# Kernel tuning notes

Hardware: AMD Instinct MI355X
Metric: run time of the kernel (lower is better)

The kernel has to match this reference:

```python
import jax, jax.numpy as jnp
import numpy as np
from jax import lax

NEG = -1e16  # value used by masked_fill in the original
DN = ('NCHW', 'OIHW', 'NCHW')


def _time_block(X, w1, b1, w2, b2, w3, b3):
    # X: [B, N, T, C] -> conv over time with kernel (1,3), VALID -> [B, N, T-2, O]
    x = jnp.transpose(X, (0, 3, 1, 2))  # [B, C, N, T]
    conv = lambda w, b: lax.conv_general_dilated(x, w, (1, 1), 'VALID', dimension_numbers=DN) + b[None, :, None, None]
    temp = conv(w1, b1) + jax.nn.sigmoid(conv(w2, b2))
    out = jax.nn.relu(temp + conv(w3, b3))
    return jnp.transpose(out, (0, 2, 3, 1))  # [B, N, T-2, O]


def _gat_single(x, graph, W, b):
    # x: [B, N, C]; W: [D, C]; b: [D]
    h = jnp.einsum('bnc,dc->bnd', x, W)
    s = jnp.einsum('bnd,bmd->bnm', h, h) * graph[None]
    s = jnp.where(s == 0, NEG, s)
    a = jax.nn.softmax(s, axis=-1)
    return jnp.einsum('bnm,bmd->bnd', a, h) + b


def _gat_multihead(x, graph, Wh, bh):
    # x: [B, N, C]; Wh: [H, D, C]; bh: [H, D] -> [B, N, H*D] (head-major concat, matching torch.cat)
    h = jnp.einsum('bnc,hdc->bhnd', x, Wh)
    s = jnp.einsum('bhnd,bhmd->bhnm', h, h) * graph[None, None]
    s = jnp.where(s == 0, NEG, s)
    a = jax.nn.softmax(s, axis=-1)
    o = jnp.einsum('bhnm,bhmd->bhnd', a, h) + bh[None, :, None, :]
    B, H, N, D = o.shape
    return jnp.transpose(o, (0, 2, 1, 3)).reshape(B, N, H * D)


def setup_inputs() -> dict:
    key = jax.random.key(0)
    ks = jax.random.split(key, 12)
    B, N, T, C = 2, 4096, 5, 192
    hid, out_c, H = 64, 64, 4
    inp = {
        'flow': jax.random.normal(ks[0], (B, N, T, C), jnp.float32),
        'graph': jax.random.randint(ks[1], (N, N), 0, 2).astype(jnp.float32),
        'tb_w1': jax.random.normal(ks[2], (hid, C, 1, 3), jnp.float32) * 0.1,
        'tb_b1': jax.random.normal(ks[3], (hid,), jnp.float32) * 0.1,
        'tb_w2': jax.random.normal(ks[4], (hid, C, 1, 3), jnp.float32) * 0.1,
        'tb_b2': jax.random.normal(ks[5], (hid,), jnp.float32) * 0.1,
        'tb_w3': jax.random.normal(ks[6], (hid, C, 1, 3), jnp.float32) * 0.1,
        'tb_b3': jax.random.normal(ks[7], (hid,), jnp.float32) * 0.1,
        'Wh': jax.random.normal(ks[8], (H, hid, C), jnp.float32) * 0.1,
        'bh': jax.random.normal(ks[9], (H, hid), jnp.float32) * 0.1,
        'Wo': jax.random.normal(ks[10], (out_c, hid * H), jnp.float32) * 0.1,
        'bo': jax.random.normal(ks[11], (out_c,), jnp.float32) * 0.1,
    }
    return inp


def reference(flow, graph, tb_w1, tb_b1, tb_w2, tb_b2, tb_w3, tb_b3, Wh, bh, Wo, bo):
    B, N = flow.shape[0], flow.shape[1]
    t1 = _time_block(flow, tb_w1, tb_b1, tb_w2, tb_b2, tb_w3, tb_b3)  # [B, N, T-2, hid]
    x = t1.reshape(B, N, -1)  # [B, N, (T-2)*hid]
    x = jax.nn.leaky_relu(_gat_multihead(x, graph, Wh, bh), negative_slope=0.01)
    x = jax.nn.leaky_relu(_gat_single(x, graph, Wo, bo), negative_slope=0.01)
    return x[:, :, None, :]  # [B, N, 1, out_c]
```

## Files before the change

kernel.cpp:

```cpp
#include <hip/hip_runtime.h>
#include <math.h>

#define N_NODES 4096

typedef unsigned short u16;
typedef unsigned int u32;

typedef __attribute__((ext_vector_type(8))) short bfrag;
typedef __attribute__((ext_vector_type(4))) float f4;

__device__ __forceinline__ u16 f2bf(float x) {
    union { float f; u32 u; } v; v.f = x;
    u32 r = (v.u + 0x7FFFu + ((v.u >> 16) & 1u)) >> 16;
    return (u16)r;
}
__device__ __forceinline__ float bf2f(u16 b) {
    union { float f; u32 u; } v; v.u = ((u32)b) << 16; return v.f;
}
__device__ __forceinline__ u32 cvtpk(float a, float b) {
    u32 r;
    asm("v_cvt_pk_bf16_f32 %0, %1, %2" : "=v"(r) : "v"(a), "v"(b));
    return r;
}
__device__ __forceinline__ float u2f(u32 u) {
    union { u32 u; float f; } v; v.u = u; return v.f;
}
__device__ __forceinline__ float fexp2(float x) {
    float r;
    asm("v_exp_f32 %0, %1" : "=v"(r) : "v"(x));
    return r;
}

#define LOG2E 1.4426950408889634f

__global__ __launch_bounds__(256) void wprep_kernel(
    const float* __restrict__ w1, const float* __restrict__ w2,
    const float* __restrict__ w3,
    u16* __restrict__ w_hi, u16* __restrict__ w_mid, u16* __restrict__ w_lo)
{
    int idx = blockIdx.x * 256 + threadIdx.x;
    if (idx >= 192 * 576) return;
    int col = idx / 576, k = idx % 576;
    int conv = col >> 6, o = col & 63;
    int kk = k / 192, c = k % 192;
    const float* w = (conv == 0) ? w1 : (conv == 1 ? w2 : w3);
    float v = w[(o * 192 + c) * 3 + kk];
    u16 h = f2bf(v);   float r1 = v - bf2f(h);
    u16 m = f2bf(r1);  float r2 = r1 - bf2f(m);
    u16 lo = f2bf(r2);
    int kc = k >> 6, rem = k & 63, j = rem >> 3, e = rem & 7;
    int pos = col * 576 + kc * 64 + ((j ^ (col & 7)) << 3) + e;
    w_hi[pos] = h;
    w_mid[pos] = m;
    w_lo[pos] = lo;
}

__global__ __launch_bounds__(512) void timeblock_mfma_kernel(
    const float* __restrict__ flow,
    const u16* __restrict__ w_hi, const u16* __restrict__ w_mid,
    const u16* __restrict__ w_lo,
    const float* __restrict__ b1, const float* __restrict__ b2,
    const float* __restrict__ b3, float* __restrict__ x1)
{
    __shared__ __align__(16) u16 As[3][128 * 64];
    __shared__ __align__(16) u16 Bs[3][192 * 64];

    const int tid = threadIdx.x;
    const int wv = tid >> 6, l = tid & 63;
    const int ln15 = l & 15, ln16 = l >> 4;
    const int wr = wv >> 1, wc = wv & 1;
    const int nodebase = blockIdx.x * 128;
    const int t = blockIdx.y;

    f4 acc[2][6];
#pragma unroll
    for (int rq = 0; rq < 2; ++rq)
#pragma unroll
        for (int nt = 0; nt < 6; ++nt) {
            acc[rq][nt][0] = 0.f; acc[rq][nt][1] = 0.f;
            acc[rq][nt][2] = 0.f; acc[rq][nt][3] = 0.f;
        }

    for (int kc = 0; kc < 9; ++kc) {
        __syncthreads();

#pragma unroll
        for (int u = tid; u < 1024; u += 512) {
            int r = u >> 3, j = u & 7;
            const float* srcp = flow + (size_t)(nodebase + r) * 960 + t * 192 + kc * 64 + j * 8;
            float4 f0 = *(const float4*)srcp;
            float4 f1 = *(const float4*)(srcp + 4);
            float fv[8] = { f0.x, f0.y, f0.z, f0.w, f1.x, f1.y, f1.z, f1.w };
            union { uint4 q; u16 a[8]; } uh, um, ul;
#pragma unroll
            for (int e = 0; e < 8; ++e) {
                u16 h = f2bf(fv[e]);   float r1 = fv[e] - bf2f(h);
                u16 m = f2bf(r1);      float r2 = r1 - bf2f(m);
                uh.a[e] = h; um.a[e] = m; ul.a[e] = f2bf(r2);
            }
            int pos = r * 64 + ((j ^ (r & 7)) << 3);
            *(uint4*)&As[0][pos] = uh.q;
            *(uint4*)&As[1][pos] = um.q;
            *(uint4*)&As[2][pos] = ul.q;
        }

#pragma unroll
        for (int arr = 0; arr < 3; ++arr) {
            const u16* wsrc = (arr == 0) ? w_hi : (arr == 1 ? w_mid : w_lo);
#pragma unroll
            for (int i = 0; i < 3; ++i) {
                int colg = wv * 24 + i * 8;
                const u16* srcp = wsrc + (size_t)(colg + (l >> 3)) * 576 + kc * 64 + (l & 7) * 8;
                u16* dstp = &Bs[arr][colg * 64];
                __builtin_amdgcn_global_load_lds(
                    (const __attribute__((address_space(1))) u32*)srcp,
                    (__attribute__((address_space(3))) u32*)dstp, 16, 0, 0);
            }
        }

        __syncthreads();

        bfrag af[2][3][2];
#pragma unroll
        for (int rq = 0; rq < 2; ++rq) {
            int arow = wr * 32 + rq * 16 + ln15;
#pragma unroll
            for (int ks = 0; ks < 2; ++ks) {
                int idx = arow * 64 + (((ks * 4 + ln16) ^ (arow & 7)) << 3);
                af[rq][0][ks] = *(const bfrag*)&As[0][idx];
                af[rq][1][ks] = *(const bfrag*)&As[1][idx];
                af[rq][2][ks] = *(const bfrag*)&As[2][idx];
            }
        }

#pragma unroll
        for (int cv = 0; cv < 3; ++cv) {
#pragma unroll
            for (int ntj = 0; ntj < 2; ++ntj) {
                int col = cv * 64 + wc * 32 + ntj * 16 + ln15;
                int nt = cv * 2 + ntj;
#pragma unroll
                for (int ks = 0; ks < 2; ++ks) {
                    int idx = col * 64 + (((ks * 4 + ln16) ^ (col & 7)) << 3);
                    bfrag bh = *(const bfrag*)&Bs[0][idx];
                    bfrag bm = *(const bfrag*)&Bs[1][idx];
                    bfrag bl = *(const bfrag*)&Bs[2][idx];
#pragma unroll
                    for (int rq = 0; rq < 2; ++rq) {
                        f4 a = acc[rq][nt];
                        a = __builtin_amdgcn_mfma_f32_16x16x32_bf16(af[rq][0][ks], bh, a, 0, 0, 0);
                        a = __builtin_amdgcn_mfma_f32_16x16x32_bf16(af[rq][0][ks], bm, a, 0, 0, 0);
                        a = __builtin_amdgcn_mfma_f32_16x16x32_bf16(af[rq][1][ks], bh, a, 0, 0, 0);
                        a = __builtin_amdgcn_mfma_f32_16x16x32_bf16(af[rq][0][ks], bl, a, 0, 0, 0);
                        a = __builtin_amdgcn_mfma_f32_16x16x32_bf16(af[rq][2][ks], bh, a, 0, 0, 0);
                        a = __builtin_amdgcn_mfma_f32_16x16x32_bf16(af[rq][1][ks], bm, a, 0, 0, 0);
                        acc[rq][nt] = a;
                    }
                }
            }
        }
    }

#pragma unroll
    for (int rq = 0; rq < 2; ++rq) {
#pragma unroll
        for (int ntj = 0; ntj < 2; ++ntj) {
            int o = wc * 32 + ntj * 16 + ln15;
            float bb1 = b1[o], bb2 = b2[o], bb3 = b3[o];
#pragma unroll
            for (int rg = 0; rg < 4; ++rg) {
                int node = nodebase + wr * 32 + rq * 16 + ln16 * 4 + rg;
                float c1 = acc[rq][0 * 2 + ntj][rg] + bb1;
                float c2 = acc[rq][1 * 2 + ntj][rg] + bb2;
                float c3 = acc[rq][2 * 2 + ntj][rg] + bb3;
                float sg = 1.0f / (1.0f + __expf(-c2));
                float v = c1 + sg + c3;
                x1[(size_t)node * 192 + t * 64 + o] = v > 0.f ? v : 0.f;
            }
        }
    }
}

__global__ __launch_bounds__(256) void linear64_split_kernel(
    const float* __restrict__ in, const float* __restrict__ W,
    u16* __restrict__ h_hi, u16* __restrict__ h_lo,
    u16* __restrict__ hTb_hi, u16* __restrict__ hTb_lo,
    int C, int H)
{
    __shared__ float xs[64][68];
    __shared__ float wsm[64][68];
    const int tid = threadIdx.x;
    const int g = blockIdx.y;
    const int rowbase = blockIdx.x * 64;
    const int rgrp = tid >> 4, cgrp = tid & 15;

    float acc[4][4] = {};
    for (int c0 = 0; c0 < C; c0 += 64) {
        __syncthreads();
        for (int i = tid; i < 4096; i += 256) {
            int r = i >> 6, cc = i & 63;
            xs[r][cc]  = in[(size_t)(rowbase + r) * C + c0 + cc];
            wsm[r][cc] = W[(size_t)(g * 64 + r) * C + c0 + cc];
        }
        __syncthreads();
        for (int cc = 0; cc < 64; cc += 4) {
            float4 xv[4], wv[4];
#pragma unroll
            for (int i = 0; i < 4; ++i)
                xv[i] = *reinterpret_cast<const float4*>(&xs[4 * rgrp + i][cc]);
#pragma unroll
            for (int j = 0; j < 4; ++j)
                wv[j] = *reinterpret_cast<const float4*>(&wsm[4 * cgrp + j][cc]);
#pragma unroll
            for (int i = 0; i < 4; ++i) {
#pragma unroll
                for (int j = 0; j < 4; ++j) {
                    acc[i][j] += xv[i].x * wv[j].x + xv[i].y * wv[j].y
                               + xv[i].z * wv[j].z + xv[i].w * wv[j].w;
                }
            }
        }
    }

    u16 hi[4][4], lo[4][4];
#pragma unroll
    for (int i = 0; i < 4; ++i)
#pragma unroll
        for (int j = 0; j < 4; ++j) {
            float a = acc[i][j];
            u16 h = f2bf(a);
            hi[i][j] = h;
            lo[i][j] = f2bf(a - bf2f(h));
        }

    const int b = rowbase >> 12;
    const size_t mapb = (size_t)(b * H + g) * (4096 * 64);

#pragma unroll
    for (int i = 0; i < 4; ++i) {
        int n = (rowbase & 4095) + 4 * rgrp + i;
        ushort4 vh = { hi[i][0], hi[i][1], hi[i][2], hi[i][3] };
        ushort4 vl = { lo[i][0], lo[i][1], lo[i][2], lo[i][3] };
        *(ushort4*)&h_hi[mapb + (size_t)n * 64 + 4 * cgrp] = vh;
        *(ushort4*)&h_lo[mapb + (size_t)n * 64 + 4 * cgrp] = vl;
    }
    {
        int n0 = (rowbase & 4095) + 4 * rgrp;
        size_t tb = mapb + ((size_t)(n0 >> 6) * 64) * 64;
#pragma unroll
        for (int j = 0; j < 4; ++j) {
            int d = 4 * cgrp + j;
            ushort4 vh = { hi[0][j], hi[1][j], hi[2][j], hi[3][j] };
            ushort4 vl = { lo[0][j], lo[1][j], lo[2][j], lo[3][j] };
            *(ushort4*)&hTb_hi[tb + (size_t)d * 64 + (n0 & 63)] = vh;
            *(ushort4*)&hTb_lo[tb + (size_t)d * 64 + (n0 & 63)] = vl;
        }
    }
}

__global__ __launch_bounds__(256) void flash_mfma_kernel(
    const u16* __restrict__ h_hi, const u16* __restrict__ h_lo,
    const u16* __restrict__ hTb_hi, const u16* __restrict__ hTb_lo,
    const float* __restrict__ graph, const float* __restrict__ bias,
    float* __restrict__ out, int H, int rstride,
    int ntiles, int nch, int mode, float* __restrict__ pO, float* __restrict__ pml)
{
    __shared__ __align__(16) u16 Ks[2][2][4096];
    __shared__ __align__(16) u16 Vs[2][4096];

    const int tid = threadIdx.x;
    const int wv = tid >> 6;
    const int l = tid & 63;
    const int ln15 = l & 15, ln16 = l >> 4;
    const int bx = blockIdx.y;
    const int by = bx / nch;
    const int chunk = bx - by * nch;
    const int t0 = chunk * ntiles;
    const int bb = by / H, head = by - bb * H;
    const size_t mapb = (size_t)by * (4096 * 64);
    const int rowbase = blockIdx.x * 64;

    const int arow = rowbase + wv * 16 + ln15;
    bfrag ahi[2], alo[2];
#pragma unroll
    for (int ks = 0; ks < 2; ++ks) {
        ahi[ks] = *(const bfrag*)(h_hi + mapb + (size_t)arow * 64 + ks * 32 + ln16 * 8);
        alo[ks] = *(const bfrag*)(h_lo + mapb + (size_t)arow * 64 + ks * 32 + ln16 * 8);
    }

    const u16* gA = (wv == 0 ? h_hi : wv == 1 ? h_lo : wv == 2 ? hTb_hi : hTb_lo) + mapb;
    const int lrow = l >> 3;
    const int stoff = lrow * 64 + (((l & 7) ^ lrow) << 3);

#define STAGE_K(T, BUF)                                                        \
    if (wv < 2) {                                                              \
        const u16* srcp = gA + (size_t)(T) * 4096 + stoff;                     \
        u16* dstp = &Ks[BUF][wv][0];                                           \
        _Pragma("unroll")                                                      \
        for (int i_ = 0; i_ < 8; ++i_)                                         \
            __builtin_amdgcn_global_load_lds(                                  \
                (const __attribute__((address_space(1))) u32*)(srcp + i_ * 512), \
                (__attribute__((address_space(3))) u32*)(dstp + i_ * 512),     \
                16, 0, 0);                                                     \
    }
#define STAGE_V(T)                                                             \
    if (wv >= 2) {                                                             \
        const u16* srcp = gA + (size_t)(T) * 4096 + stoff;                     \
        u16* dstp = &Vs[wv - 2][0];                                            \
        _Pragma("unroll")                                                      \
        for (int i_ = 0; i_ < 8; ++i_)                                         \
            __builtin_amdgcn_global_load_lds(                                  \
                (const __attribute__((address_space(1))) u32*)(srcp + i_ * 512), \
                (__attribute__((address_space(3))) u32*)(dstp + i_ * 512),     \
                16, 0, 0);                                                     \
    }

    const float* grow = graph + (size_t)(rowbase + wv * 16 + ln15) * 4096 + ln16 * 4;

    float m_ = -3.0e38f, l_ = 0.f;
    f4 acco[4];
#pragma unroll
    for (int i = 0; i < 4; ++i) {
        acco[i][0] = 0.f; acco[i][1] = 0.f; acco[i][2] = 0.f; acco[i][3] = 0.f;
    }

    STAGE_K(t0, 0);
    float4 grC[4], grN[4];
#pragma unroll
    for (int cb = 0; cb < 4; ++cb)
        grC[cb] = *(const float4*)(grow + (size_t)t0 * 64 + cb * 16);

    const int srcA = ln15 + ((((ln16 << 1)) & 3) << 4);
    const int srcB = ln15 + ((((ln16 << 1) + 1) & 3) << 4);
    const bool hi2 = (ln16 & 2) != 0;

    for (int tt = 0; tt < ntiles; ++tt) {
        const int t = t0 + tt;
        const int cur = tt & 1;

        __syncthreads();

        STAGE_V(t);
        if (tt + 1 < ntiles) {
            STAGE_K(t + 1, cur ^ 1);
#pragma unroll
            for (int cb = 0; cb < 4; ++cb)
                grN[cb] = *(const float4*)(grow + (size_t)(t + 1) * 64 + cb * 16);
        }

        __builtin_amdgcn_s_setprio(1);
        f4 accs[4];
#pragma unroll
        for (int cb = 0; cb < 4; ++cb) {
            f4 a; a[0] = 0.f; a[1] = 0.f; a[2] = 0.f; a[3] = 0.f;
#pragma unroll
            for (int ks = 0; ks < 2; ++ks) {
                int c = cb * 16 + ln15;
                int idx = c * 64 + (((ks * 4 + ln16) * 8) ^ ((c & 7) << 3));
                bfrag bhi = *(const bfrag*)&Ks[cur][0][idx];
                bfrag blo = *(const bfrag*)&Ks[cur][1][idx];
                a = __builtin_amdgcn_mfma_f32_16x16x32_bf16(bhi, ahi[ks], a, 0, 0, 0);
                a = __builtin_amdgcn_mfma_f32_16x16x32_bf16(bhi, alo[ks], a, 0, 0, 0);
                a = __builtin_amdgcn_mfma_f32_16x16x32_bf16(blo, ahi[ks], a, 0, 0, 0);
            }
            accs[cb] = a;
        }
        __builtin_amdgcn_s_setprio(0);

        float p[4][4];
#pragma unroll
        for (int cb = 0; cb < 4; ++cb) {
            p[cb][0] = accs[cb][0] + fmaf(grC[cb].x, 1e16f, -1e16f);
            p[cb][1] = accs[cb][1] + fmaf(grC[cb].y, 1e16f, -1e16f);
            p[cb][2] = accs[cb][2] + fmaf(grC[cb].z, 1e16f, -1e16f);
            p[cb][3] = accs[cb][3] + fmaf(grC[cb].w, 1e16f, -1e16f);
        }

        float tm = fmaxf(fmaxf(p[0][0], p[0][1]), fmaxf(p[0][2], p[0][3]));
#pragma unroll
        for (int cb = 1; cb < 4; ++cb)
            tm = fmaxf(tm, fmaxf(fmaxf(p[cb][0], p[cb][1]), fmaxf(p[cb][2], p[cb][3])));
        tm = fmaxf(tm, __shfl_xor(tm, 16));
        tm = fmaxf(tm, __shfl_xor(tm, 32));

        const bool anyup = __any(tm > m_);
        float mn, corr;
        if (anyup) {
            mn = fmaxf(m_, tm);
            corr = fexp2((m_ - mn) * LOG2E);
        } else {
            mn = m_;
            corr = 1.0f;
        }
        const float c0 = -mn * LOG2E;

        float rs = 0.f;
#pragma unroll
        for (int cb = 0; cb < 4; ++cb) {
            p[cb][0] = fexp2(fmaf(p[cb][0], LOG2E, c0));
            p[cb][1] = fexp2(fmaf(p[cb][1], LOG2E, c0));
            p[cb][2] = fexp2(fmaf(p[cb][2], LOG2E, c0));
            p[cb][3] = fexp2(fmaf(p[cb][3], LOG2E, c0));
            rs += (p[cb][0] + p[cb][1]) + (p[cb][2] + p[cb][3]);
        }
        rs += __shfl_xor(rs, 16);
        rs += __shfl_xor(rs, 32);
        l_ = l_ * corr + rs;
        m_ = mn;

        if (anyup) {
            float corr4[4];
#pragma unroll
            for (int rg = 0; rg < 4; ++rg)
                corr4[rg] = __shfl(corr, ln16 * 4 + rg);
#pragma unroll
            for (int nb = 0; nb < 4; ++nb) {
                acco[nb][0] *= corr4[0]; acco[nb][1] *= corr4[1];
                acco[nb][2] *= corr4[2]; acco[nb][3] *= corr4[3];
            }
        }

        u32 Uh[4][2], Ul[4][2];
#pragma unroll
        for (int cb = 0; cb < 4; ++cb) {
            u32 uh0 = cvtpk(p[cb][0], p[cb][1]);
            u32 uh1 = cvtpk(p[cb][2], p[cb][3]);
            float h0 = u2f(uh0 << 16), h1 = u2f(uh0 & 0xffff0000u);
            float h2 = u2f(uh1 << 16), h3 = u2f(uh1 & 0xffff0000u);
            Uh[cb][0] = uh0; Uh[cb][1] = uh1;
            Ul[cb][0] = cvtpk(p[cb][0] - h0, p[cb][1] - h1);
            Ul[cb][1] = cvtpk(p[cb][2] - h2, p[cb][3] - h3);
        }

        bfrag pfh[2], pfl[2];
#pragma unroll
        for (int ks = 0; ks < 2; ++ks) {
            u32 w0a = (u32)__shfl((int)Uh[2 * ks + 0][0], srcA);
            u32 w0b = (u32)__shfl((int)Uh[2 * ks + 1][0], srcA);
            u32 w1a = (u32)__shfl((int)Uh[2 * ks + 0][1], srcA);
            u32 w1b = (u32)__shfl((int)Uh[2 * ks + 1][1], srcA);
            u32 w2a = (u32)__shfl((int)Uh[2 * ks + 0][0], srcB);
            u32 w2b = (u32)__shfl((int)Uh[2 * ks + 1][0], srcB);
            u32 w3a = (u32)__shfl((int)Uh[2 * ks + 0][1], srcB);
            u32 w3b = (u32)__shfl((int)Uh[2 * ks + 1][1], srcB);
            union { uint4 q; bfrag f; } ch;
            ch.q.x = hi2 ? w0b : w0a; ch.q.y = hi2 ? w1b : w1a;
            ch.q.z = hi2 ? w2b : w2a; ch.q.w = hi2 ? w3b : w3a;
            pfh[ks] = ch.f;

            u32 v0a = (u32)__shfl((int)Ul[2 * ks + 0][0], srcA);
            u32 v0b = (u32)__shfl((int)Ul[2 * ks + 1][0], srcA);
            u32 v1a = (u32)__shfl((int)Ul[2 * ks + 0][1], srcA);
            u32 v1b = (u32)__shfl((int)Ul[2 * ks + 1][1], srcA);
            u32 v2a = (u32)__shfl((int)Ul[2 * ks + 0][0], srcB);
            u32 v2b = (u32)__shfl((int)Ul[2 * ks + 1][0], srcB);
            u32 v3a = (u32)__shfl((int)Ul[2 * ks + 0][1], srcB);
            u32 v3b = (u32)__shfl((int)Ul[2 * ks + 1][1], srcB);
            union { uint4 q; bfrag f; } cl;
            cl.q.x = hi2 ? v0b : v0a; cl.q.y = hi2 ? v1b : v1a;
            cl.q.z = hi2 ? v2b : v2a; cl.q.w = hi2 ? v3b : v3a;
            pfl[ks] = cl.f;
        }

        __syncthreads();

        __builtin_amdgcn_s_setprio(1);
#pragma unroll
        for (int nb = 0; nb < 4; ++nb) {
#pragma unroll
            for (int ks = 0; ks < 2; ++ks) {
                int nr = nb * 16 + ln15;
                int idx = nr * 64 + (((ks * 4 + ln16) * 8) ^ ((nr & 7) << 3));
                bfrag vhi = *(const bfrag*)&Vs[0][idx];
                bfrag vlo = *(const bfrag*)&Vs[1][idx];
                acco[nb] = __builtin_amdgcn_mfma_f32_16x16x32_bf16(pfh[ks], vhi, acco[nb], 0, 0, 0);
                acco[nb] = __builtin_amdgcn_mfma_f32_16x16x32_bf16(pfh[ks], vlo, acco[nb], 0, 0, 0);
                acco[nb] = __builtin_amdgcn_mfma_f32_16x16x32_bf16(pfl[ks], vhi, acco[nb], 0, 0, 0);
            }
        }
        __builtin_amdgcn_s_setprio(0);

        if (tt + 1 < ntiles) {
#pragma unroll
            for (int cb = 0; cb < 4; ++cb)
                grC[cb] = grN[cb];
        }
    }
#undef STAGE_K
#undef STAGE_V

    if (mode == 0) {
        float l4[4];
#pragma unroll
        for (int rg = 0; rg < 4; ++rg)
            l4[rg] = __shfl(l_, ln16 * 4 + rg);

        const float* bv = bias + head * 64;
#pragma unroll
        for (int rg = 0; rg < 4; ++rg) {
            int row = rowbase + wv * 16 + ln16 * 4 + rg;
            float inv = 1.0f / l4[rg];
#pragma unroll
            for (int nb = 0; nb < 4; ++nb) {
                float v = acco[nb][rg] * inv + bv[nb * 16 + ln15];
                v = v > 0.f ? v : 0.01f * v;
                out[(size_t)(bb * N_NODES + row) * rstride + head * 64 + nb * 16 + ln15] = v;
            }
        }
    } else {
        int row = rowbase + wv * 16 + ln15;
        if (ln16 == 0) {
            size_t mi = (((size_t)(by * nch + chunk)) * 4096 + row) * 2;
            pml[mi] = m_;
            pml[mi + 1] = l_;
        }
#pragma unroll
        for (int rg = 0; rg < 4; ++rg) {
            int row2 = rowbase + wv * 16 + ln16 * 4 + rg;
            size_t ob = (((size_t)(by * nch + chunk)) * 4096 + row2) * 64;
#pragma unroll
            for (int nb = 0; nb < 4; ++nb)
                pO[ob + nb * 16 + ln15] = acco[nb][rg];
        }
    }
}

__global__ __launch_bounds__(256) void merge_kernel(
    const float* __restrict__ pO, const float* __restrict__ pml,
    const float* __restrict__ bias, float* __restrict__ out)
{
    int idx = blockIdx.x * 256 + threadIdx.x;
    int feat = idx & 63;
    int row = (idx >> 6) & 4095;
    int map = idx >> 18;

    float mv[4], lv[4];
    float M = -3.0e38f;
#pragma unroll
    for (int c = 0; c < 4; ++c) {
        size_t mi = (((size_t)map * 4 + c) * 4096 + row) * 2;
        mv[c] = pml[mi];
        lv[c] = pml[mi + 1];
        M = fmaxf(M, mv[c]);
    }
    float den = 0.f, num = 0.f;
#pragma unroll
    for (int c = 0; c < 4; ++c) {
        float e = __expf(mv[c] - M);
        den += e * lv[c];
        num += e * pO[(((size_t)map * 4 + c) * 4096 + row) * 64 + feat];
    }
    float v = num / den + bias[feat];
    v = v > 0.f ? v : 0.01f * v;
    out[((size_t)map * 4096 + row) * 64 + feat] = v;
}

extern "C" void kernel_launch(void* const* d_in, const int* in_sizes, int n_in,
                              void* d_out, int out_size, void* d_ws, size_t ws_size,
                              hipStream_t stream)
{
    const float* flow = (const float*)d_in[0];
    const float* graph = (const float*)d_in[1];
    const float* w1 = (const float*)d_in[2];
    const float* b1 = (const float*)d_in[3];
    const float* w2 = (const float*)d_in[4];
    const float* b2 = (const float*)d_in[5];
    const float* w3 = (const float*)d_in[6];
    const float* b3 = (const float*)d_in[7];
    const float* Wh = (const float*)d_in[8];
    const float* bh = (const float*)d_in[9];
    const float* Wo = (const float*)d_in[10];
    const float* bo = (const float*)d_in[11];

    char* ws = (char*)d_ws;
    u16* wc_hi  = (u16*)ws;
    u16* wc_mid = wc_hi + (size_t)192 * 576;
    u16* wc_lo  = wc_mid + (size_t)192 * 576;

    u16* h1_hi  = (u16*)ws;
    u16* h1_lo  = h1_hi + (size_t)8 * 4096 * 64;
    u16* h1T_hi = h1_lo + (size_t)8 * 4096 * 64;
    u16* h1T_lo = h1T_hi + (size_t)8 * 4096 * 64;
    u16* h2_hi  = (u16*)ws;
    u16* h2_lo  = h2_hi + (size_t)2 * 4096 * 64;
    u16* h2T_hi = h2_lo + (size_t)2 * 4096 * 64;
    u16* h2T_lo = h2T_hi + (size_t)2 * 4096 * 64;
    float* pml  = (float*)(ws + (size_t)6 * 1024 * 1024);
    float* xreg = (float*)(ws + (size_t)4 * 8 * 4096 * 64 * 2);
    float* x1 = xreg;
    float* x2 = xreg;
    float* pO = xreg;
    float* outp = (float*)d_out;

    hipLaunchKernelGGL(wprep_kernel, dim3(432), dim3(256), 0, stream,
                       w1, w2, w3, wc_hi, wc_mid, wc_lo);
    hipLaunchKernelGGL(timeblock_mfma_kernel, dim3(64, 3), dim3(512), 0, stream,
                       flow, wc_hi, wc_mid, wc_lo, b1, b2, b3, x1);
    hipLaunchKernelGGL(linear64_split_kernel, dim3(128, 4), dim3(256), 0, stream,
                       x1, Wh, h1_hi, h1_lo, h1T_hi, h1T_lo, 192, 4);
    hipLaunchKernelGGL(flash_mfma_kernel, dim3(64, 8), dim3(256), 0, stream,
                       h1_hi, h1_lo, h1T_hi, h1T_lo, graph, bh, x2, 4, 256,
                       64, 1, 0, (float*)nullptr, (float*)nullptr);
    hipLaunchKernelGGL(linear64_split_kernel, dim3(128, 1), dim3(256), 0, stream,
                       x2, Wo, h2_hi, h2_lo, h2T_hi, h2T_lo, 256, 1);
    hipLaunchKernelGGL(flash_mfma_kernel, dim3(64, 8), dim3(256), 0, stream,
                       h2_hi, h2_lo, h2T_hi, h2T_lo, graph, bo, (float*)nullptr, 1, 64,
                       16, 4, 1, pO, pml);
    hipLaunchKernelGGL(merge_kernel, dim3(2048), dim3(256), 0, stream,
                       pO, pml, bo, outp);
}
```

Measured before the change: 313.7 us.

## Replace scalar FP32 linear projection with 3-way split bf16 MFMA GEMM

```diff
diff --git a/kernel.cpp b/kernel.cpp
--- a/kernel.cpp
+++ b/kernel.cpp
@@ -181,77 +181,140 @@
     }
 }
 
-__global__ __launch_bounds__(256) void linear64_split_kernel(
+__global__ __launch_bounds__(512) void linear_mfma_kernel(
     const float* __restrict__ in, const float* __restrict__ W,
     u16* __restrict__ h_hi, u16* __restrict__ h_lo,
     u16* __restrict__ hTb_hi, u16* __restrict__ hTb_lo,
-    int C, int H)
+    int C, int H, int nwc)
 {
-    __shared__ float xs[64][68];
-    __shared__ float wsm[64][68];
+    __shared__ __align__(16) u16 As[3][256 * 64];
+    __shared__ __align__(16) u16 Bs[3][128 * 64];
+
     const int tid = threadIdx.x;
-    const int g = blockIdx.y;
-    const int rowbase = blockIdx.x * 64;
-    const int rgrp = tid >> 4, cgrp = tid & 15;
-
-    float acc[4][4] = {};
-    for (int c0 = 0; c0 < C; c0 += 64) {
+    const int wv = tid >> 6, l = tid & 63;
+    const int ln15 = l & 15, ln16 = l >> 4;
+    const int wr = wv / nwc, wc = wv - wr * nwc;
+    const int rows = 256 / nwc;
+    const int ncol = 64 * nwc;
+    const int rowbase = blockIdx.x * rows;
+    const int colbase = blockIdx.y * ncol;
+
+    f4 acc[2][4];
+#pragma unroll
+    for (int rq = 0; rq < 2; ++rq)
+#pragma unroll
+        for (int nt = 0; nt < 4; ++nt) {
+            acc[rq][nt][0] = 0.f; acc[rq][nt][1] = 0.f;
+            acc[rq][nt][2] = 0.f; acc[rq][nt][3] = 0.f;
+        }
+
+    const int nchunks = C >> 6;
+    for (int kc = 0; kc < nchunks; ++kc) {
         __syncthreads();
-        for (int i = tid; i < 4096; i += 256) {
-            int r = i >> 6, cc = i & 63;
-            xs[r][cc]  = in[(size_t)(rowbase + r) * C + c0 + cc];
-            wsm[r][cc] = W[(size_t)(g * 64 + r) * C + c0 + cc];
-        }
+
+        for (int u = tid; u < rows * 8; u += 512) {
+            int r = u >> 3, j = u & 7;
+            const float* srcp = in + (size_t)(rowbase + r) * C + kc * 64 + j * 8;
+            float4 f0 = *(const float4*)srcp;
+            float4 f1 = *(const float4*)(srcp + 4);
+            float fv[8] = { f0.x, f0.y, f0.z, f0.w, f1.x, f1.y, f1.z, f1.w };
+            union { uint4 q; u16 a[8]; } uh, um, ul;
+#pragma unroll
+            for (int e = 0; e < 8; ++e) {
+                u16 h = f2bf(fv[e]);   float r1 = fv[e] - bf2f(h);
+                u16 m = f2bf(r1);      float r2 = r1 - bf2f(m);
+                uh.a[e] = h; um.a[e] = m; ul.a[e] = f2bf(r2);
+            }
+            int pos = r * 64 + ((j ^ (r & 7)) << 3);
+            *(uint4*)&As[0][pos] = uh.q;
+            *(uint4*)&As[1][pos] = um.q;
+            *(uint4*)&As[2][pos] = ul.q;
+        }
+
+        for (int u = tid; u < ncol * 8; u += 512) {
+            int cdx = u >> 3, j = u & 7;
+            const float* srcp = W + (size_t)(colbase + cdx) * C + kc * 64 + j * 8;
+            float4 f0 = *(const float4*)srcp;
+            float4 f1 = *(const float4*)(srcp + 4);
+            float fv[8] = { f0.x, f0.y, f0.z, f0.w, f1.x, f1.y, f1.z, f1.w };
+            union { uint4 q; u16 a[8]; } uh, um, ul;
+#pragma unroll
+            for (int e = 0; e < 8; ++e) {
+                u16 h = f2bf(fv[e]);   float r1 = fv[e] - bf2f(h);
+                u16 m = f2bf(r1);      float r2 = r1 - bf2f(m);
+                uh.a[e] = h; um.a[e] = m; ul.a[e] = f2bf(r2);
+            }
+            int pos = cdx * 64 + ((j ^ (cdx & 7)) << 3);
+            *(uint4*)&Bs[0][pos] = uh.q;
+            *(uint4*)&Bs[1][pos] = um.q;
+            *(uint4*)&Bs[2][pos] = ul.q;
+        }
+
         __syncthreads();
-        for (int cc = 0; cc < 64; cc += 4) {
-            float4 xv[4], wv[4];
-#pragma unroll
-            for (int i = 0; i < 4; ++i)
-                xv[i] = *reinterpret_cast<const float4*>(&xs[4 * rgrp + i][cc]);
-#pragma unroll
-            for (int j = 0; j < 4; ++j)
-                wv[j] = *reinterpret_cast<const float4*>(&wsm[4 * cgrp + j][cc]);
-#pragma unroll
-            for (int i = 0; i < 4; ++i) {
-#pragma unroll
-                for (int j = 0; j < 4; ++j) {
-                    acc[i][j] += xv[i].x * wv[j].x + xv[i].y * wv[j].y
-                               + xv[i].z * wv[j].z + xv[i].w * wv[j].w;
+
+        bfrag af[2][3][2];
+#pragma unroll
+        for (int rq = 0; rq < 2; ++rq) {
+            int arow = wr * 32 + rq * 16 + ln15;
+#pragma unroll
+            for (int ks = 0; ks < 2; ++ks) {
+                int idx = arow * 64 + (((ks * 4 + ln16) ^ (arow & 7)) << 3);
+                af[rq][0][ks] = *(const bfrag*)&As[0][idx];
+                af[rq][1][ks] = *(const bfrag*)&As[1][idx];
+                af[rq][2][ks] = *(const bfrag*)&As[2][idx];
+            }
+        }
+
+#pragma unroll
+        for (int nt = 0; nt < 4; ++nt) {
+            int bcol = wc * 64 + nt * 16 + ln15;
+#pragma unroll
+            for (int ks = 0; ks < 2; ++ks) {
+                int idx = bcol * 64 + (((ks * 4 + ln16) ^ (bcol & 7)) << 3);
+                bfrag bh = *(const bfrag*)&Bs[0][idx];
+                bfrag bm = *(const bfrag*)&Bs[1][idx];
+                bfrag bl = *(const bfrag*)&Bs[2][idx];
+#pragma unroll
+                for (int rq = 0; rq < 2; ++rq) {
+                    f4 a = acc[rq][nt];
+                    a = __builtin_amdgcn_mfma_f32_16x16x32_bf16(af[rq][0][ks], bh, a, 0, 0, 0);
+                    a = __builtin_amdgcn_mfma_f32_16x16x32_bf16(af[rq][0][ks], bm, a, 0, 0, 0);
+                    a = __builtin_amdgcn_mfma_f32_16x16x32_bf16(af[rq][1][ks], bh, a, 0, 0, 0);
+                    a = __builtin_amdgcn_mfma_f32_16x16x32_bf16(af[rq][0][ks], bl, a, 0, 0, 0);
+                    a = __builtin_amdgcn_mfma_f32_16x16x32_bf16(af[rq][2][ks], bh, a, 0, 0, 0);
+                    a = __builtin_amdgcn_mfma_f32_16x16x32_bf16(af[rq][1][ks], bm, a, 0, 0, 0);
+                    acc[rq][nt] = a;
                 }
             }
         }
     }
 
-    u16 hi[4][4], lo[4][4];
-#pragma unroll
-    for (int i = 0; i < 4; ++i)
-#pragma unroll
-        for (int j = 0; j < 4; ++j) {
-            float a = acc[i][j];
-            u16 h = f2bf(a);
-            hi[i][j] = h;
-            lo[i][j] = f2bf(a - bf2f(h));
-        }
-
-    const int b = rowbase >> 12;
-    const size_t mapb = (size_t)(b * H + g) * (4096 * 64);
-
-#pragma unroll
-    for (int i = 0; i < 4; ++i) {
-        int n = (rowbase & 4095) + 4 * rgrp + i;
-        ushort4 vh = { hi[i][0], hi[i][1], hi[i][2], hi[i][3] };
-        ushort4 vl = { lo[i][0], lo[i][1], lo[i][2], lo[i][3] };
-        *(ushort4*)&h_hi[mapb + (size_t)n * 64 + 4 * cgrp] = vh;
-        *(ushort4*)&h_lo[mapb + (size_t)n * 64 + 4 * cgrp] = vl;
-    }
-    {
-        int n0 = (rowbase & 4095) + 4 * rgrp;
-        size_t tb = mapb + ((size_t)(n0 >> 6) * 64) * 64;
-#pragma unroll
-        for (int j = 0; j < 4; ++j) {
-            int d = 4 * cgrp + j;
-            ushort4 vh = { hi[0][j], hi[1][j], hi[2][j], hi[3][j] };
-            ushort4 vl = { lo[0][j], lo[1][j], lo[2][j], lo[3][j] };
+#pragma unroll
+    for (int rq = 0; rq < 2; ++rq) {
+#pragma unroll
+        for (int nt = 0; nt < 4; ++nt) {
+            int col = colbase + wc * 64 + nt * 16 + ln15;
+            int g = col >> 6, d = col & 63;
+            u16 hi4[4], lo4[4];
+#pragma unroll
+            for (int rg = 0; rg < 4; ++rg) {
+                float a = acc[rq][nt][rg];
+                u16 h = f2bf(a);
+                hi4[rg] = h;
+                lo4[rg] = f2bf(a - bf2f(h));
+            }
+            int row0 = rowbase + wr * 32 + rq * 16 + ln16 * 4;
+            int b = row0 >> 12;
+            int n0 = row0 & 4095;
+            size_t mapb = (size_t)(b * H + g) * (4096 * 64);
+#pragma unroll
+            for (int rg = 0; rg < 4; ++rg) {
+                h_hi[mapb + (size_t)(n0 + rg) * 64 + d] = hi4[rg];
+                h_lo[mapb + (size_t)(n0 + rg) * 64 + d] = lo4[rg];
+            }
+            size_t tb = mapb + (size_t)(n0 >> 6) * 4096;
+            ushort4 vh = { hi4[0], hi4[1], hi4[2], hi4[3] };
+            ushort4 vl = { lo4[0], lo4[1], lo4[2], lo4[3] };
             *(ushort4*)&hTb_hi[tb + (size_t)d * 64 + (n0 & 63)] = vh;
             *(ushort4*)&hTb_lo[tb + (size_t)d * 64 + (n0 & 63)] = vl;
         }
@@ -596,13 +659,13 @@
                        w1, w2, w3, wc_hi, wc_mid, wc_lo);
     hipLaunchKernelGGL(timeblock_mfma_kernel, dim3(64, 3), dim3(512), 0, stream,
                        flow, wc_hi, wc_mid, wc_lo, b1, b2, b3, x1);
-    hipLaunchKernelGGL(linear64_split_kernel, dim3(128, 4), dim3(256), 0, stream,
-                       x1, Wh, h1_hi, h1_lo, h1T_hi, h1T_lo, 192, 4);
+    hipLaunchKernelGGL(linear_mfma_kernel, dim3(64, 2), dim3(512), 0, stream,
+                       x1, Wh, h1_hi, h1_lo, h1T_hi, h1T_lo, 192, 4, 2);
     hipLaunchKernelGGL(flash_mfma_kernel, dim3(64, 8), dim3(256), 0, stream,
                        h1_hi, h1_lo, h1T_hi, h1T_lo, graph, bh, x2, 4, 256,
                        64, 1, 0, (float*)nullptr, (float*)nullptr);
-    hipLaunchKernelGGL(linear64_split_kernel, dim3(128, 1), dim3(256), 0, stream,
-                       x2, Wo, h2_hi, h2_lo, h2T_hi, h2T_lo, 256, 1);
+    hipLaunchKernelGGL(linear_mfma_kernel, dim3(32, 1), dim3(512), 0, stream,
+                       x2, Wo, h2_hi, h2_lo, h2T_hi, h2T_lo, 256, 1, 1);
     hipLaunchKernelGGL(flash_mfma_kernel, dim3(64, 8), dim3(256), 0, stream,
                        h2_hi, h2_lo, h2T_hi, h2T_lo, graph, bo, (float*)nullptr, 1, 64,
                        16, 4, 1, pO, pml);
```

Result: faster. 303.7 us (median of 2 runs) (-3.2%).
